# Optimization experiments

Hardware: AMD Instinct MI355X
Metric: run time of the kernel (lower is better)

Reference implementation:

```python
import jax, jax.numpy as jnp
import numpy as np

B, S, H, G, W = 4, 4096, 1024, 256, 8
CHUNK = 1024
NUM_HEADS = 4


def _ln(x, g, b, eps=1e-5):
    m = jnp.mean(x, axis=-1, keepdims=True)
    v = jnp.var(x, axis=-1, keepdims=True)
    return (x - m) / jnp.sqrt(v + eps) * g + b


def setup_inputs() -> dict:
    key = jax.random.key(0)
    ks = jax.random.split(key, 16)
    Hm = H // 2
    return {
        "x": jax.random.normal(ks[0], (B, S, H), dtype=jnp.float32),
        # wavelet params
        "mother_wavelets": jax.random.normal(ks[1], (1, W, H, 1), dtype=jnp.float32) * 0.02,
        "scales": jnp.ones((1, W, 1, 1), dtype=jnp.float32),
        # coeff_mixer: Linear(W,H/2) -> LN -> GELU -> Linear(H/2,H)  (weights stored as (in,out))
        "mix_w1": jax.random.normal(ks[2], (W, Hm), dtype=jnp.float32) * 0.02,
        "mix_b1": jnp.zeros((Hm,), dtype=jnp.float32),
        "mix_ln_g": jnp.ones((Hm,), dtype=jnp.float32),
        "mix_ln_b": jnp.zeros((Hm,), dtype=jnp.float32),
        "mix_w2": jax.random.normal(ks[3], (Hm, H), dtype=jnp.float32) * 0.02,
        "mix_b2": jnp.zeros((H,), dtype=jnp.float32),
        # attention (no bias)
        "wq": jax.random.normal(ks[4], (H, H), dtype=jnp.float32) * 0.02,
        "wk": jax.random.normal(ks[5], (H, H), dtype=jnp.float32) * 0.02,
        "wv": jax.random.normal(ks[6], (H, H), dtype=jnp.float32) * 0.02,
        "wo": jax.random.normal(ks[7], (H, H), dtype=jnp.float32) * 0.02,
        # output_proj: LN -> Linear(H, G)
        "out_ln_g": jnp.ones((H,), dtype=jnp.float32),
        "out_ln_b": jnp.zeros((H,), dtype=jnp.float32),
        "out_w": jax.random.normal(ks[8], (H, G), dtype=jnp.float32) * 0.02,
        "out_b": jnp.zeros((G,), dtype=jnp.float32),
    }


def reference(x, mother_wavelets, scales, mix_w1, mix_b1, mix_ln_g, mix_ln_b,
              mix_w2, mix_b2, wq, wk, wv, wo, out_ln_g, out_ln_b, out_w, out_b):
    b, s, h = x.shape
    nc = s // CHUNK  # chunks are independent -> fold into batch
    xc = x.reshape(b * nc, CHUNK, h)

    # wavelet coeffs: conv1d with kernel length == channels reduces to a dot product
    norm = jnp.sqrt(jnp.sum(mother_wavelets ** 2, axis=2, keepdims=True))
    kern = (mother_wavelets / jnp.maximum(norm, 1e-12)) * jax.nn.sigmoid(scales)
    kern = kern[0, :, :, 0]  # (W, H)
    coeffs = jnp.einsum('bsh,wh->bsw', xc, kern)  # (b*nc, L, W)

    # coeff mixer
    hid = _ln(coeffs @ mix_w1 + mix_b1, mix_ln_g, mix_ln_b)
    mixed = jax.nn.gelu(hid, approximate=False) @ mix_w2 + mix_b2  # (b*nc, L, H)

    # multi-head attention within each chunk (eval mode -> no causal mask)
    hd = h // NUM_HEADS
    def heads(t):
        return t.reshape(-1, CHUNK, NUM_HEADS, hd).transpose(0, 2, 1, 3)
    q, k, v = heads(mixed @ wq), heads(mixed @ wk), heads(mixed @ wv)
    scores = jnp.einsum('bhqd,bhkd->bhqk', q, k) * (hd ** -0.5)
    attn = jax.nn.softmax(scores, axis=-1)
    o = jnp.einsum('bhqk,bhkd->bhqd', attn, v)
    o = o.transpose(0, 2, 1, 3).reshape(-1, CHUNK, h) @ wo

    # output projection with residual
    y = _ln(o + mixed, out_ln_g, out_ln_b) @ out_w + out_b  # (b*nc, L, G)
    return y.reshape(b, s, -1)
```

## Files before the change

### kernel.cpp

```cpp
#include <hip/hip_runtime.h>
#include <hip/hip_bf16.h>

typedef __bf16 bf16;
typedef __bf16 bf16x4 __attribute__((ext_vector_type(4)));
typedef __bf16 bf16x8 __attribute__((ext_vector_type(8)));
typedef float f32x4 __attribute__((ext_vector_type(4)));
typedef unsigned short ushort8_t __attribute__((ext_vector_type(8)));
typedef unsigned int u32x2 __attribute__((ext_vector_type(2)));

#define GLOAD_LDS16(g, l)                                                      \
    __builtin_amdgcn_global_load_lds(                                          \
        (const __attribute__((address_space(1))) void*)(g),                    \
        (__attribute__((address_space(3))) void*)(l), 16, 0, 0)

#define LDS_ADDR(p) ((unsigned)(uintptr_t)(__attribute__((address_space(3))) void*)(p))


__global__ __launch_bounds__(256) void k_wavelet(const float* __restrict__ mw,
                                                 const float* __restrict__ sc,
                                                 float* __restrict__ kern) {
    int w = blockIdx.x;
    int tid = threadIdx.x;
    float s = 0.f;
    for (int h = tid; h < 1024; h += 256) { float v = mw[w * 1024 + h]; s += v * v; }
#pragma unroll
    for (int xm = 1; xm < 64; xm <<= 1) s += __shfl_xor(s, xm);
    __shared__ float red[4];
    if ((tid & 63) == 0) red[tid >> 6] = s;
    __syncthreads();
    float tot = red[0] + red[1] + red[2] + red[3];
    float inv = 1.f / fmaxf(sqrtf(tot), 1e-12f);
    float sg = 1.f / (1.f + __expf(-sc[w]));
    float m = inv * sg;
    for (int h = tid; h < 1024; h += 256) kern[w * 1024 + h] = mw[w * 1024 + h] * m;
}

__global__ __launch_bounds__(256) void k_coeffs(const float* __restrict__ x,
                                                const float* __restrict__ kern,
                                                float* __restrict__ coeffs) {
    __shared__ float kl[8 * 1024];
    int tid = threadIdx.x;
    for (int i = tid; i < 8192; i += 256) kl[i] = kern[i];
    __syncthreads();
    int wid = tid >> 6, lane = tid & 63;
    long row = (long)blockIdx.x * 4 + wid;
    float acc[8] = {0, 0, 0, 0, 0, 0, 0, 0};
    const float* xr = x + row * 1024;
    for (int i = 0; i < 16; i++) {
        float xv = xr[lane + i * 64];
#pragma unroll
        for (int w = 0; w < 8; w++) acc[w] += xv * kl[w * 1024 + lane + i * 64];
    }
#pragma unroll
    for (int xm = 1; xm < 64; xm <<= 1) {
#pragma unroll
        for (int w = 0; w < 8; w++) acc[w] += __shfl_xor(acc[w], xm);
    }
    if (lane == 0) {
#pragma unroll
        for (int w = 0; w < 8; w++) coeffs[row * 8 + w] = acc[w];
    }
}

__global__ __launch_bounds__(256) void k_mix1(const float* __restrict__ coeffs,
                                              const float* __restrict__ w1,
                                              const float* __restrict__ b1,
                                              const float* __restrict__ lng,
                                              const float* __restrict__ lnb,
                                              bf16* __restrict__ g) {
    long row = blockIdx.x;
    int tid = threadIdx.x;
    int wid = tid >> 6, lane = tid & 63;
    __shared__ float cf[8];
    __shared__ float red1[4], red2[4];
    if (tid < 8) cf[tid] = coeffs[row * 8 + tid];
    __syncthreads();
    float h0[2];
#pragma unroll
    for (int t = 0; t < 2; t++) {
        int j = tid + t * 256;
        float a = b1[j];
#pragma unroll
        for (int w = 0; w < 8; w++) a += cf[w] * w1[w * 512 + j];
        h0[t] = a;
    }
    float s1 = h0[0] + h0[1];
    float s2 = h0[0] * h0[0] + h0[1] * h0[1];
#pragma unroll
    for (int xm = 1; xm < 64; xm <<= 1) {
        s1 += __shfl_xor(s1, xm);
        s2 += __shfl_xor(s2, xm);
    }
    if (lane == 0) { red1[wid] = s1; red2[wid] = s2; }
    __syncthreads();
    s1 = red1[0] + red1[1] + red1[2] + red1[3];
    s2 = red2[0] + red2[1] + red2[2] + red2[3];
    float mean = s1 * (1.f / 512.f);
    float var = s2 * (1.f / 512.f) - mean * mean;
    float inv = rsqrtf(var + 1e-5f);
#pragma unroll
    for (int t = 0; t < 2; t++) {
        int j = tid + t * 256;
        float xn = (h0[t] - mean) * inv * lng[j] + lnb[j];
        float ge = 0.5f * xn * (1.f + erff(xn * 0.70710678118654752f));
        g[row * 512 + j] = (bf16)ge;
    }
}

__global__ void k_wtrans_all(const float* __restrict__ w2, const float* __restrict__ wq,
                             const float* __restrict__ wk, const float* __restrict__ wv,
                             const float* __restrict__ wo, const float* __restrict__ ow,
                             bf16* __restrict__ w2t, bf16* __restrict__ wqt,
                             bf16* __restrict__ wkt, bf16* __restrict__ wvt,
                             bf16* __restrict__ wot, bf16* __restrict__ owt) {
    long idx = (long)blockIdx.x * 256 + threadIdx.x;
    if (idx < 524288) {
        int kk = (int)(idx >> 10), n = (int)(idx & 1023);
        w2t[(long)n * 512 + kk] = (bf16)w2[idx];
    } else if (idx < 4718592) {
        long r = idx - 524288;
        int m = (int)(r >> 20);
        long q = r & 1048575;
        int kk = (int)(q >> 10), n = (int)(q & 1023);
        const float* src = (m == 0) ? wq : (m == 1) ? wk : (m == 2) ? wv : wo;
        bf16* dst = (m == 0) ? wqt : (m == 1) ? wkt : (m == 2) ? wvt : wot;
        dst[(long)n * 1024 + kk] = (bf16)src[q];
    } else {
        long r = idx - 4718592;
        int kk = (int)(r >> 8), n = (int)(r & 255);
        owt[(long)n * 1024 + kk] = (bf16)ow[r];
    }
}

enum { EPI_BF16 = 0, EPI_BF16_BIAS = 1, EPI_F32_BIAS = 2, EPI_VT = 3, EPI_F32 = 4 };

template <int EPI>
__global__ __launch_bounds__(512, 2) void k_gemm256(const bf16* __restrict__ A,
                                                    const bf16* __restrict__ Bt,
                                                    const float* __restrict__ bias,
                                                    void* __restrict__ Cout,
                                                    int K, int lda, int ldb, int ldc,
                                                    float scale) {
    __shared__ bf16 As[2 * 256 * 64];
    __shared__ bf16 Bs[2 * 256 * 64];
    int tid = threadIdx.x;
    int wid = tid >> 6, lane = tid & 63;
    int wr = wid >> 2, wc = wid & 3;
    long m0 = (long)blockIdx.y * 256, n0 = (long)blockIdx.x * 256;
    f32x4 acc[8][4] = {};
    const int lr = lane & 15, ko = (lane >> 4) << 3;

    const int grow = wid * 8 + (lane >> 3);
    const int gcol = (lane & 7) << 3;
    const bf16* aS = A + (m0 + grow) * lda + gcol;
    const bf16* bS = Bt + (n0 + grow) * ldb + gcol;
    bf16* lA = As + wid * 512;
    bf16* lB = Bs + wid * 512;

    const int nt = K >> 6;
#pragma unroll
    for (int i = 0; i < 4; i++) {
        GLOAD_LDS16(aS + (long)(i * 64) * lda, lA + i * 4096);
        GLOAD_LDS16(bS + (long)(i * 64) * ldb, lB + i * 4096);
    }
    __syncthreads();
    int buf = 0;
    for (int t = 0; t < nt; t++) {
        if (t + 1 < nt) {
            const int k0 = (t + 1) << 6;
            const int ob = (buf ^ 1) << 14;
#pragma unroll
            for (int i = 0; i < 4; i++) {
                GLOAD_LDS16(aS + (long)(i * 64) * lda + k0, lA + ob + i * 4096);
                GLOAD_LDS16(bS + (long)(i * 64) * ldb + k0, lB + ob + i * 4096);
            }
        }
        const bf16* At = As + (buf << 14);
        const bf16* Bb = Bs + (buf << 14);
#pragma unroll
        for (int kk = 0; kk < 2; kk++) {
            bf16x8 af[8], bfr[4];
#pragma unroll
            for (int i = 0; i < 8; i++)
                af[i] = *(const bf16x8*)&At[(wr * 128 + i * 16 + lr) * 64 + kk * 32 + ko];
#pragma unroll
            for (int j = 0; j < 4; j++)
                bfr[j] = *(const bf16x8*)&Bb[(wc * 64 + j * 16 + lr) * 64 + kk * 32 + ko];
#pragma unroll
            for (int i = 0; i < 8; i++) {
#pragma unroll
                for (int j = 0; j < 4; j++)
                    acc[i][j] = __builtin_amdgcn_mfma_f32_16x16x32_bf16(af[i], bfr[j], acc[i][j], 0, 0, 0);
            }
        }
        __syncthreads();
        buf ^= 1;
    }
    const int r0 = (lane >> 4) << 2;
#pragma unroll
    for (int i = 0; i < 8; i++) {
#pragma unroll
        for (int j = 0; j < 4; j++) {
#pragma unroll
            for (int e = 0; e < 4; e++) {
                long m = m0 + wr * 128 + i * 16 + r0 + e;
                long n = n0 + wc * 64 + j * 16 + lr;
                float v = acc[i][j][e] * scale;
                if constexpr (EPI == EPI_BF16_BIAS || EPI == EPI_F32_BIAS) v += bias[n];
                if constexpr (EPI == EPI_F32_BIAS || EPI == EPI_F32) {
                    ((float*)Cout)[m * ldc + n] = v;
                } else if constexpr (EPI == EPI_VT) {
                    long c = m >> 10, s = m & 1023, h = n >> 8, d = n & 255;
                    ((bf16*)Cout)[(((c << 2) + h) << 18) + (d << 10) + s] = (bf16)v;
                } else {
                    ((bf16*)Cout)[m * ldc + n] = (bf16)v;
                }
            }
        }
    }
}

template <int EPI>
__global__ __launch_bounds__(256) void k_gemm(const bf16* __restrict__ A,
                                              const bf16* __restrict__ Bt,
                                              const float* __restrict__ bias,
                                              void* __restrict__ Cout,
                                              int M, int N, int K,
                                              int lda, int ldb, int ldc, float scale) {
    __shared__ bf16 As[128 * 32];
    __shared__ bf16 Bs[128 * 32];
    int tid = threadIdx.x;
    int wid = tid >> 6, lane = tid & 63;
    int wr = wid >> 1, wc = wid & 1;
    long m0 = (long)blockIdx.y * 128, n0 = (long)blockIdx.x * 128;
    f32x4 acc[4][4] = {};
    const int lr = lane & 15, ko = (lane >> 4) << 3;

    const int srow = wid * 32 + (lane >> 2);
    const int scol = (lane & 3) << 3;
    const bf16* a0 = A + (m0 + srow) * lda + scol;
    const bf16* a1 = A + (m0 + srow + 16) * lda + scol;
    const bf16* b0 = Bt + (n0 + srow) * ldb + scol;
    const bf16* b1 = Bt + (n0 + srow + 16) * ldb + scol;
    bf16* la0 = As + wid * 1024;
    bf16* la1 = As + wid * 1024 + 512;
    bf16* lb0 = Bs + wid * 1024;
    bf16* lb1 = Bs + wid * 1024 + 512;

    for (int k0 = 0; k0 < K; k0 += 32) {
        GLOAD_LDS16(a0 + k0, la0);
        GLOAD_LDS16(a1 + k0, la1);
        GLOAD_LDS16(b0 + k0, lb0);
        GLOAD_LDS16(b1 + k0, lb1);
        __syncthreads();
        bf16x8 af[4], bfr[4];
#pragma unroll
        for (int i = 0; i < 4; i++)
            af[i] = *(const bf16x8*)&As[(wr * 64 + i * 16 + lr) * 32 + ko];
#pragma unroll
        for (int i = 0; i < 4; i++)
            bfr[i] = *(const bf16x8*)&Bs[(wc * 64 + i * 16 + lr) * 32 + ko];
#pragma unroll
        for (int i = 0; i < 4; i++) {
#pragma unroll
            for (int j = 0; j < 4; j++)
                acc[i][j] = __builtin_amdgcn_mfma_f32_16x16x32_bf16(af[i], bfr[j], acc[i][j], 0, 0, 0);
        }
        __syncthreads();
    }
    const int r0 = (lane >> 4) << 2;
#pragma unroll
    for (int i = 0; i < 4; i++) {
#pragma unroll
        for (int j = 0; j < 4; j++) {
#pragma unroll
            for (int e = 0; e < 4; e++) {
                long m = m0 + wr * 64 + i * 16 + r0 + e;
                long n = n0 + wc * 64 + j * 16 + lr;
                float v = acc[i][j][e] * scale;
                if constexpr (EPI == EPI_BF16_BIAS || EPI == EPI_F32_BIAS) v += bias[n];
                if constexpr (EPI == EPI_F32_BIAS || EPI == EPI_F32) {
                    ((float*)Cout)[m * ldc + n] = v;
                } else if constexpr (EPI == EPI_VT) {
                    long c = m >> 10, s = m & 1023, h = n >> 8, d = n & 255;
                    ((bf16*)Cout)[(((c << 2) + h) << 18) + (d << 10) + s] = (bf16)v;
                } else {
                    ((bf16*)Cout)[m * ldc + n] = (bf16)v;
                }
            }
        }
    }
}

__global__ __launch_bounds__(512, 2) void k_attn(const bf16* __restrict__ q,
                                                 const bf16* __restrict__ k,
                                                 const bf16* __restrict__ vt,
                                                 bf16* __restrict__ ao) {
    __shared__ __align__(16) bf16 smem[2 * 16384 + 2 * 16384 + 8192];
    bf16* Ks = smem;
    bf16* Vs = smem + 32768;
    bf16* Ps = smem + 65536;
    int tid = threadIdx.x;
    int wid = tid >> 6, lane = tid & 63;
    int c = blockIdx.x, h = blockIdx.y, q0 = blockIdx.z * 128;
    const int lr = lane & 15, gq = lane >> 4, ko = gq << 3;
    const int l7 = lr & 7;

    const int krw = wid * 2 + (lane >> 5);
    const int kg = (lane & 31) ^ (krw & 7);
    const bf16* ksrc = k + ((long)c << 10) * 1024 + h * 256 + kg * 8;
    const int vrw = wid * 8 + ((lane >> 3) & 7);
    const int vg = (lane & 7) ^ ((lane >> 3) & 7);
    const bf16* vsrc = vt + ((long)(c * 4 + h) << 18) + vg * 8;

    long qrow = ((long)c << 10) + q0 + wid * 16 + lr;
    bf16x8 qf[8];
#pragma unroll
    for (int kk = 0; kk < 8; kk++)
        qf[kk] = *(const bf16x8*)&q[qrow * 1024 + h * 256 + kk * 32 + ko];

    f32x4 oacc[16] = {};
    float m_run[4] = {-1e30f, -1e30f, -1e30f, -1e30f};
    float l_run[4] = {0.f, 0.f, 0.f, 0.f};

    bf16* PT = Ps + (wid << 10);
    const unsigned pva = LDS_ADDR(&PT[(gq << 7) + lr]);

#pragma unroll
    for (int i = 0; i < 4; i++) {
        GLOAD_LDS16(ksrc + (long)(i * 16 + krw) * 1024, Ks + i * 4096 + wid * 512);
        GLOAD_LDS16(vsrc + (long)(i * 64 + vrw) * 1024, Vs + i * 4096 + wid * 512);
    }
    __syncthreads();
    int buf = 0;
    for (int t = 0; t < 16; t++) {
        if (t < 15) {
            const int kb = (t + 1) << 6;
            const int ob = (buf ^ 1) << 14;
#pragma unroll
            for (int i = 0; i < 4; i++) {
                GLOAD_LDS16(ksrc + (long)(kb + i * 16 + krw) * 1024, Ks + ob + i * 4096 + wid * 512);
                GLOAD_LDS16(vsrc + (long)(i * 64 + vrw) * 1024 + kb, Vs + ob + i * 4096 + wid * 512);
            }
        }
        const bf16* Kc = Ks + (buf << 14);
        const bf16* Vc = Vs + (buf << 14);
        f32x4 s[4] = {};
        __builtin_amdgcn_s_setprio(1);
#pragma unroll
        for (int kk = 0; kk < 8; kk++) {
#pragma unroll
            for (int n = 0; n < 4; n++)
                s[n] = __builtin_amdgcn_mfma_f32_16x16x32_bf16(
                    qf[kk],
                    *(const bf16x8*)&Kc[((n * 16 + lr) << 8) + ((((kk << 2) + gq) ^ l7) << 3)],
                    s[n], 0, 0, 0);
        }
        __builtin_amdgcn_s_setprio(0);
        float mx[4];
#pragma unroll
        for (int e = 0; e < 4; e++)
            mx[e] = fmaxf(fmaxf(s[0][e], s[1][e]), fmaxf(s[2][e], s[3][e]));
#pragma unroll
        for (int xm = 1; xm < 16; xm <<= 1) {
#pragma unroll
            for (int e = 0; e < 4; e++) mx[e] = fmaxf(mx[e], __shfl_xor(mx[e], xm));
        }
        bool need = (mx[0] > m_run[0] + 8.f) || (mx[1] > m_run[1] + 8.f) ||
                    (mx[2] > m_run[2] + 8.f) || (mx[3] > m_run[3] + 8.f);
        if (__any(need)) {
#pragma unroll
            for (int e = 0; e < 4; e++) {
                float mn = fmaxf(m_run[e], mx[e]);
                float al = __expf(m_run[e] - mn);
                m_run[e] = mn;
                l_run[e] *= al;
#pragma unroll
                for (int f = 0; f < 16; f++) oacc[f][e] *= al;
            }
        }
        float rs[4] = {0.f, 0.f, 0.f, 0.f};
#pragma unroll
        for (int n = 0; n < 4; n++) {
#pragma unroll
            for (int e = 0; e < 4; e++) {
                float p = __expf(s[n][e] - m_run[e]);
                s[n][e] = p;
                rs[e] += p;
            }
        }
#pragma unroll
        for (int xm = 1; xm < 16; xm <<= 1) {
#pragma unroll
            for (int e = 0; e < 4; e++) rs[e] += __shfl_xor(rs[e], xm);
        }
#pragma unroll
        for (int e = 0; e < 4; e++) l_run[e] += rs[e];
#pragma unroll
        for (int n = 0; n < 4; n++) {
            bf16x4 pv = {(bf16)s[n][0], (bf16)s[n][1], (bf16)s[n][2], (bf16)s[n][3]};
            *(bf16x4*)&PT[((n * 16 + lr) << 4) + (gq << 2)] = pv;
        }
        asm volatile("s_waitcnt lgkmcnt(0)" ::: "memory");
        u32x2 t0, t1, t2, t3;
        asm volatile("ds_read_b64_tr_b16 %0, %1" : "=v"(t0) : "v"(pva));
        asm volatile("ds_read_b64_tr_b16 %0, %1 offset:128" : "=v"(t1) : "v"(pva));
        asm volatile("ds_read_b64_tr_b16 %0, %1 offset:1024" : "=v"(t2) : "v"(pva));
        asm volatile("ds_read_b64_tr_b16 %0, %1 offset:1152" : "=v"(t3) : "v"(pva));
        asm volatile("s_waitcnt lgkmcnt(0)" ::: "memory");
        __builtin_amdgcn_sched_barrier(0);
        union { u32x2 u[2]; bf16x8 v; } p0, p1;
        p0.u[0] = t0; p0.u[1] = t1;
        p1.u[0] = t2; p1.u[1] = t3;
        const bf16x8 pf0 = p0.v, pf1 = p1.v;
        __builtin_amdgcn_s_setprio(1);
#pragma unroll
        for (int n2 = 0; n2 < 16; n2++) {
            const int vrow = (n2 * 16 + lr) << 6;
            const int vswz = gq ^ l7;
            oacc[n2] = __builtin_amdgcn_mfma_f32_16x16x32_bf16(
                pf0, *(const bf16x8*)&Vc[vrow + (vswz << 3)], oacc[n2], 0, 0, 0);
            oacc[n2] = __builtin_amdgcn_mfma_f32_16x16x32_bf16(
                pf1, *(const bf16x8*)&Vc[vrow + ((vswz ^ 4) << 3)], oacc[n2], 0, 0, 0);
        }
        __builtin_amdgcn_s_setprio(0);
        __syncthreads();
        buf ^= 1;
    }
#pragma unroll
    for (int n2 = 0; n2 < 16; n2++) {
#pragma unroll
        for (int e = 0; e < 4; e++) {
            long row = ((long)c << 10) + q0 + wid * 16 + (gq << 2) + e;
            long col = ((long)h << 8) + n2 * 16 + lr;
            ao[row * 1024 + col] = (bf16)(oacc[n2][e] / l_run[e]);
        }
    }
}

__global__ __launch_bounds__(256) void k_outln(const bf16* __restrict__ o,
                                               const bf16* __restrict__ mixed,
                                               const float* __restrict__ g,
                                               const float* __restrict__ b,
                                               bf16* __restrict__ t) {
    long row = blockIdx.x;
    int tid = threadIdx.x;
    int wid = tid >> 6, lane = tid & 63;
    __shared__ float red1[4], red2[4];
    float x[4];
    const bf16* orow = o + row * 1024;
    const bf16* mrow = mixed + row * 1024;
    bf16x4 ov = *(const bf16x4*)&orow[tid * 4];
    bf16x4 mv = *(const bf16x4*)&mrow[tid * 4];
#pragma unroll
    for (int i = 0; i < 4; i++) x[i] = (float)ov[i] + (float)mv[i];
    float s1 = x[0] + x[1] + x[2] + x[3];
    float s2 = x[0] * x[0] + x[1] * x[1] + x[2] * x[2] + x[3] * x[3];
#pragma unroll
    for (int xm = 1; xm < 64; xm <<= 1) {
        s1 += __shfl_xor(s1, xm);
        s2 += __shfl_xor(s2, xm);
    }
    if (lane == 0) { red1[wid] = s1; red2[wid] = s2; }
    __syncthreads();
    s1 = red1[0] + red1[1] + red1[2] + red1[3];
    s2 = red2[0] + red2[1] + red2[2] + red2[3];
    float mean = s1 * (1.f / 1024.f);
    float var = s2 * (1.f / 1024.f) - mean * mean;
    float inv = rsqrtf(var + 1e-5f);
#pragma unroll
    for (int i = 0; i < 4; i++) {
        int j = tid * 4 + i;
        t[row * 1024 + j] = (bf16)((x[i] - mean) * inv * g[j] + b[j]);
    }
}

extern "C" void kernel_launch(void* const* d_in, const int* in_sizes, int n_in,
                              void* d_out, int out_size, void* d_ws, size_t ws_size,
                              hipStream_t stream) {
    const float* x   = (const float*)d_in[0];
    const float* mw  = (const float*)d_in[1];
    const float* sc  = (const float*)d_in[2];
    const float* w1  = (const float*)d_in[3];
    const float* b1  = (const float*)d_in[4];
    const float* lng1 = (const float*)d_in[5];
    const float* lnb1 = (const float*)d_in[6];
    const float* w2  = (const float*)d_in[7];
    const float* b2  = (const float*)d_in[8];
    const float* wq  = (const float*)d_in[9];
    const float* wk  = (const float*)d_in[10];
    const float* wv  = (const float*)d_in[11];
    const float* wo  = (const float*)d_in[12];
    const float* lng2 = (const float*)d_in[13];
    const float* lnb2 = (const float*)d_in[14];
    const float* ow  = (const float*)d_in[15];
    const float* ob  = (const float*)d_in[16];

    char* p = (char*)d_ws;
    auto take = [&](size_t bytes) {
        char* r = p;
        p += (bytes + 255) & ~(size_t)255;
        return r;
    };
    const size_t M = 16384;
    float* kern   = (float*)take(8 * 1024 * sizeof(float));
    float* coeffs = (float*)take(M * 8 * sizeof(float));
    bf16* g       = (bf16*)take(M * 512 * 2);
    bf16* mixed   = (bf16*)take(M * 1024 * 2);
    bf16* qb      = (bf16*)take(M * 1024 * 2 * 2);
    bf16* kb2     = qb + M * 1024;
    bf16* obf     = qb;
    bf16* vtb     = (bf16*)take(M * 1024 * 2);
    bf16* tb      = vtb;
    bf16* aob     = (bf16*)take(M * 1024 * 2);
    bf16* w2t     = (bf16*)take((size_t)1024 * 512 * 2);
    bf16* wqt     = (bf16*)take((size_t)1024 * 1024 * 2);
    bf16* wkt     = (bf16*)take((size_t)1024 * 1024 * 2);
    bf16* wvt     = (bf16*)take((size_t)1024 * 1024 * 2);
    bf16* wot     = (bf16*)take((size_t)1024 * 1024 * 2);
    bf16* owt     = (bf16*)take((size_t)256 * 1024 * 2);

    k_wavelet<<<8, 256, 0, stream>>>(mw, sc, kern);
    k_coeffs<<<4096, 256, 0, stream>>>(x, kern, coeffs);
    k_mix1<<<16384, 256, 0, stream>>>(coeffs, w1, b1, lng1, lnb1, g);

    k_wtrans_all<<<19456, 256, 0, stream>>>(w2, wq, wk, wv, wo, ow,
                                            w2t, wqt, wkt, wvt, wot, owt);

    k_gemm256<EPI_BF16_BIAS><<<dim3(4, 64), 512, 0, stream>>>(
        g, w2t, b2, mixed, 512, 512, 512, 1024, 1.f);
    k_gemm256<EPI_BF16><<<dim3(4, 64), 512, 0, stream>>>(
        mixed, wqt, nullptr, qb, 1024, 1024, 1024, 1024, 0.0625f);
    k_gemm256<EPI_BF16><<<dim3(4, 64), 512, 0, stream>>>(
        mixed, wkt, nullptr, kb2, 1024, 1024, 1024, 1024, 1.f);
    k_gemm256<EPI_VT><<<dim3(4, 64), 512, 0, stream>>>(
        mixed, wvt, nullptr, vtb, 1024, 1024, 1024, 1024, 1.f);
    k_attn<<<dim3(16, 4, 8), 512, 0, stream>>>(qb, kb2, vtb, aob);
    k_gemm256<EPI_BF16><<<dim3(4, 64), 512, 0, stream>>>(
        aob, wot, nullptr, obf, 1024, 1024, 1024, 1024, 1.f);
    k_outln<<<16384, 256, 0, stream>>>(obf, mixed, lng2, lnb2, tb);
    k_gemm<EPI_F32_BIAS><<<dim3(2, 128), 256, 0, stream>>>(
        tb, owt, ob, d_out, 16384, 256, 1024, 1024, 1024, 256, 1.f);
}
```

Measured before the change: 460.2 us.

## Restructure 256x256 GEMM into 8-phase pipelined schedule with swizzled LDS

Replaces the double-buffered 256x256 bf16 GEMM with an 8-phase schedule. Each phase interleaves global-to-LDS staging of half-tiles with a slice of MFMA work, using explicit barriers, waitcnts and setprio. LDS column addressing is XOR-swizzled to cut bank conflicts on fragment reads. The goal is to hide load latency behind MFMA and reduce LDS conflicts, at the cost of fragile manual scheduling and tighter assumptions about K. The leftover stray label 'GLOAAD_DUMMY:' inside a lambda looks odd but should still compile.

```diff
diff --git a/kernel.cpp b/kernel.cpp
--- a/kernel.cpp
+++ b/kernel.cpp
@@ -14,6 +14,13 @@
         (__attribute__((address_space(3))) void*)(l), 16, 0, 0)
 
 #define LDS_ADDR(p) ((unsigned)(uintptr_t)(__attribute__((address_space(3))) void*)(p))
+
+#define SBAR()                                                                 \
+    do {                                                                       \
+        __builtin_amdgcn_sched_barrier(0);                                     \
+        __builtin_amdgcn_s_barrier();                                          \
+        __builtin_amdgcn_sched_barrier(0);                                     \
+    } while (0)
 
 
 __global__ __launch_bounds__(256) void k_wavelet(const float* __restrict__ mw,
@@ -135,67 +142,140 @@
 enum { EPI_BF16 = 0, EPI_BF16_BIAS = 1, EPI_F32_BIAS = 2, EPI_VT = 3, EPI_F32 = 4 };
 
 template <int EPI>
-__global__ __launch_bounds__(512, 2) void k_gemm256(const bf16* __restrict__ A,
-                                                    const bf16* __restrict__ Bt,
-                                                    const float* __restrict__ bias,
-                                                    void* __restrict__ Cout,
-                                                    int K, int lda, int ldb, int ldc,
-                                                    float scale) {
-    __shared__ bf16 As[2 * 256 * 64];
-    __shared__ bf16 Bs[2 * 256 * 64];
-    int tid = threadIdx.x;
-    int wid = tid >> 6, lane = tid & 63;
-    int wr = wid >> 2, wc = wid & 3;
-    long m0 = (long)blockIdx.y * 256, n0 = (long)blockIdx.x * 256;
+__global__ __launch_bounds__(512, 2) void k_gemm8p(const bf16* __restrict__ A,
+                                                   const bf16* __restrict__ Bt,
+                                                   const float* __restrict__ bias,
+                                                   void* __restrict__ Cout,
+                                                   int K, int lda, int ldb, int ldc,
+                                                   float scale) {
+    __shared__ bf16 As[2 * 2 * 128 * 64];
+    __shared__ bf16 Bs[2 * 2 * 128 * 64];
+    const int tid = threadIdx.x;
+    const int wid = tid >> 6, lane = tid & 63;
+    const int wr = wid >> 2, wc = wid & 3;
+    const long m0 = (long)blockIdx.y * 256, n0 = (long)blockIdx.x * 256;
     f32x4 acc[8][4] = {};
-    const int lr = lane & 15, ko = (lane >> 4) << 3;
-
-    const int grow = wid * 8 + (lane >> 3);
-    const int gcol = (lane & 7) << 3;
-    const bf16* aS = A + (m0 + grow) * lda + gcol;
-    const bf16* bS = Bt + (n0 + grow) * ldb + gcol;
-    bf16* lA = As + wid * 512;
-    bf16* lB = Bs + wid * 512;
+    const int lr = lane & 15, gq = lane >> 4;
+    const int l7 = lr & 7;
+
+    const int srow = wid * 8 + (lane >> 3);
+    const int sg = (lane & 7) ^ (lane >> 3);
+    const bf16* aS = A + (m0 + srow) * lda + sg * 8;
+    const bf16* bS = Bt + (n0 + srow) * ldb + sg * 8;
+
+    auto stageA = [&](int t, int h) {
+        bf16* d = As + (((t & 1) * 2 + h) * 128) * 64 + wid * 512;
+        const long kq = (long)t << 6;
+        GLOAAD_DUMMY:;
+        GLOAD_LDS16(aS + (long)(h * 128) * lda + kq, d);
+        GLOAD_LDS16(aS + (long)(h * 128 + 64) * lda + kq, d + 4096);
+    };
+    auto stageB = [&](int t, int h) {
+        bf16* d = Bs + (((t & 1) * 2 + h) * 128) * 64 + wid * 512;
+        const long kq = (long)t << 6;
+        GLOAD_LDS16(bS + (long)(h * 128) * ldb + kq, d);
+        GLOAD_LDS16(bS + (long)(h * 128 + 64) * ldb + kq, d + 4096);
+    };
+
+    bf16x8 bfr[4][2];
+    auto ldB = [&](int b) {
+#pragma unroll
+        for (int j = 0; j < 4; j++)
+#pragma unroll
+            for (int kk = 0; kk < 2; kk++)
+                bfr[j][kk] = *(const bf16x8*)&Bs[((b * 2 + (wc >> 1)) * 128 +
+                                                 (wc & 1) * 64 + j * 16 + lr) * 64 +
+                                                (((kk * 4 + gq) ^ l7) << 3)];
+    };
 
     const int nt = K >> 6;
-#pragma unroll
-    for (int i = 0; i < 4; i++) {
-        GLOAD_LDS16(aS + (long)(i * 64) * lda, lA + i * 4096);
-        GLOAD_LDS16(bS + (long)(i * 64) * ldb, lB + i * 4096);
-    }
-    __syncthreads();
-    int buf = 0;
-    for (int t = 0; t < nt; t++) {
-        if (t + 1 < nt) {
-            const int k0 = (t + 1) << 6;
-            const int ob = (buf ^ 1) << 14;
-#pragma unroll
-            for (int i = 0; i < 4; i++) {
-                GLOAD_LDS16(aS + (long)(i * 64) * lda + k0, lA + ob + i * 4096);
-                GLOAD_LDS16(bS + (long)(i * 64) * ldb + k0, lB + ob + i * 4096);
+    const int niter = nt >> 1;
+
+    stageA(0, 0); stageA(0, 1); stageB(0, 0); stageB(0, 1);
+    stageB(1, 0); stageB(1, 1);
+    asm volatile("s_waitcnt vmcnt(4)" ::: "memory");
+    SBAR();
+
+    for (int jit = 0; jit < niter - 1; ++jit) {
+        const int T = jit << 1;
+#pragma unroll
+        for (int tp = 0; tp < 2; ++tp) {
+#pragma unroll
+            for (int q = 0; q < 4; ++q) {
+                bf16x8 af[2][2];
+                if (q == 0) ldB(tp);
+#pragma unroll
+                for (int ii = 0; ii < 2; ii++)
+#pragma unroll
+                    for (int kk = 0; kk < 2; kk++)
+                        af[ii][kk] = *(const bf16x8*)&As[((tp * 2 + wr) * 128 +
+                                                         (q * 2 + ii) * 16 + lr) * 64 +
+                                                        (((kk * 4 + gq) ^ l7) << 3)];
+                if (tp == 0) {
+                    if (q == 0) stageA(T + 1, 0);
+                    else if (q == 1) stageA(T + 1, 1);
+                    else if (q == 2) stageB(T + 2, 0);
+                    else stageB(T + 2, 1);
+                } else {
+                    if (q == 0) stageA(T + 2, 0);
+                    else if (q == 1) stageA(T + 2, 1);
+                    else if (q == 2) stageB(T + 3, 0);
+                    else stageB(T + 3, 1);
+                }
+                if (q == 3) asm volatile("s_waitcnt vmcnt(4)" ::: "memory");
+                SBAR();
+                asm volatile("s_waitcnt lgkmcnt(0)" ::: "memory");
+                __builtin_amdgcn_s_setprio(1);
+#pragma unroll
+                for (int ii = 0; ii < 2; ii++)
+#pragma unroll
+                    for (int j = 0; j < 4; j++) {
+                        acc[q * 2 + ii][j] = __builtin_amdgcn_mfma_f32_16x16x32_bf16(
+                            af[ii][0], bfr[j][0], acc[q * 2 + ii][j], 0, 0, 0);
+                        acc[q * 2 + ii][j] = __builtin_amdgcn_mfma_f32_16x16x32_bf16(
+                            af[ii][1], bfr[j][1], acc[q * 2 + ii][j], 0, 0, 0);
+                    }
+                __builtin_amdgcn_s_setprio(0);
+                SBAR();
             }
         }
-        const bf16* At = As + (buf << 14);
-        const bf16* Bb = Bs + (buf << 14);
-#pragma unroll
-        for (int kk = 0; kk < 2; kk++) {
-            bf16x8 af[8], bfr[4];
-#pragma unroll
-            for (int i = 0; i < 8; i++)
-                af[i] = *(const bf16x8*)&At[(wr * 128 + i * 16 + lr) * 64 + kk * 32 + ko];
-#pragma unroll
-            for (int j = 0; j < 4; j++)
-                bfr[j] = *(const bf16x8*)&Bb[(wc * 64 + j * 16 + lr) * 64 + kk * 32 + ko];
-#pragma unroll
-            for (int i = 0; i < 8; i++) {
-#pragma unroll
-                for (int j = 0; j < 4; j++)
-                    acc[i][j] = __builtin_amdgcn_mfma_f32_16x16x32_bf16(af[i], bfr[j], acc[i][j], 0, 0, 0);
+    }
+    {
+        const int T = nt - 2;
+#pragma unroll
+        for (int tp = 0; tp < 2; ++tp) {
+#pragma unroll
+            for (int q = 0; q < 4; ++q) {
+                bf16x8 af[2][2];
+                if (q == 0) ldB(tp);
+#pragma unroll
+                for (int ii = 0; ii < 2; ii++)
+#pragma unroll
+                    for (int kk = 0; kk < 2; kk++)
+                        af[ii][kk] = *(const bf16x8*)&As[((tp * 2 + wr) * 128 +
+                                                         (q * 2 + ii) * 16 + lr) * 64 +
+                                                        (((kk * 4 + gq) ^ l7) << 3)];
+                if (tp == 0 && q == 0) stageA(T + 1, 0);
+                if (tp == 0 && q == 1) stageA(T + 1, 1);
+                if (tp == 0 && q == 3) asm volatile("s_waitcnt vmcnt(0)" ::: "memory");
+                SBAR();
+                asm volatile("s_waitcnt lgkmcnt(0)" ::: "memory");
+                __builtin_amdgcn_s_setprio(1);
+#pragma unroll
+                for (int ii = 0; ii < 2; ii++)
+#pragma unroll
+                    for (int j = 0; j < 4; j++) {
+                        acc[q * 2 + ii][j] = __builtin_amdgcn_mfma_f32_16x16x32_bf16(
+                            af[ii][0], bfr[j][0], acc[q * 2 + ii][j], 0, 0, 0);
+                        acc[q * 2 + ii][j] = __builtin_amdgcn_mfma_f32_16x16x32_bf16(
+                            af[ii][1], bfr[j][1], acc[q * 2 + ii][j], 0, 0, 0);
+                    }
+                __builtin_amdgcn_s_setprio(0);
+                SBAR();
             }
         }
-        __syncthreads();
-        buf ^= 1;
-    }
+    }
+
     const int r0 = (lane >> 4) << 2;
 #pragma unroll
     for (int i = 0; i < 8; i++) {
@@ -527,16 +607,16 @@
     k_wtrans_all<<<19456, 256, 0, stream>>>(w2, wq, wk, wv, wo, ow,
                                             w2t, wqt, wkt, wvt, wot, owt);
 
-    k_gemm256<EPI_BF16_BIAS><<<dim3(4, 64), 512, 0, stream>>>(
+    k_gemm8p<EPI_BF16_BIAS><<<dim3(4, 64), 512, 0, stream>>>(
         g, w2t, b2, mixed, 512, 512, 512, 1024, 1.f);
-    k_gemm256<EPI_BF16><<<dim3(4, 64), 512, 0, stream>>>(
+    k_gemm8p<EPI_BF16><<<dim3(4, 64), 512, 0, stream>>>(
         mixed, wqt, nullptr, qb, 1024, 1024, 1024, 1024, 0.0625f);
-    k_gemm256<EPI_BF16><<<dim3(4, 64), 512, 0, stream>>>(
+    k_gemm8p<EPI_BF16><<<dim3(4, 64), 512, 0, stream>>>(
         mixed, wkt, nullptr, kb2, 1024, 1024, 1024, 1024, 1.f);
-    k_gemm256<EPI_VT><<<dim3(4, 64), 512, 0, stream>>>(
+    k_gemm8p<EPI_VT><<<dim3(4, 64), 512, 0, stream>>>(
         mixed, wvt, nullptr, vtb, 1024, 1024, 1024, 1024, 1.f);
     k_attn<<<dim3(16, 4, 8), 512, 0, stream>>>(qb, kb2, vtb, aob);
-    k_gemm256<EPI_BF16><<<dim3(4, 64), 512, 0, stream>>>(
+    k_gemm8p<EPI_BF16><<<dim3(4, 64), 512, 0, stream>>>(
         aob, wot, nullptr, obf, 1024, 1024, 1024, 1024, 1.f);
     k_outln<<<16384, 256, 0, stream>>>(obf, mixed, lng2, lnb2, tb);
     k_gemm<EPI_F32_BIAS><<<dim3(2, 128), 256, 0, stream>>>(
```

After: 431.4 us. -6.3%, faster.
